# Performance work log

Measured on AMD Instinct MI355X. Metric: run time of the kernel, lower is better.

Reference implementation:

```python
import jax, jax.numpy as jnp
import numpy as np

T_DIFF = 1000.0
LN_EPS = 1e-5


def _lin(x, w, b):
    return jnp.matmul(x, w.T) + b


def _ln(x, g, b):
    m = jnp.mean(x, axis=-1, keepdims=True)
    v = jnp.mean((x - m) ** 2, axis=-1, keepdims=True)
    return (x - m) / jnp.sqrt(v + LN_EPS) * g + b


def _pos_lin(x, w, b):
    return jnp.matmul(x, jax.nn.softplus(w).T) + b


def _gamma(t, g_l1_w, g_l1_b, g_l2_w, g_l2_b, g_l3_w, g_l3_b, gamma_0, gamma_1):
    def gtilde(u):
        l1 = _pos_lin(u, g_l1_w, g_l1_b)
        return l1 + _pos_lin(jax.nn.sigmoid(_pos_lin(l1, g_l2_w, g_l2_b)), g_l3_w, g_l3_b)
    g0, g1, gt = gtilde(jnp.zeros_like(t)), gtilde(jnp.ones_like(t)), gtilde(t)
    return gamma_0 + (gamma_1 - gamma_0) * (gt - g0) / (g1 - g0)


def _pair_dist(a):
    # safe pairwise euclidean distances, (B,N,N,1)
    diff = a[:, :, None, :] - a[:, None, :, :]
    d2 = jnp.sum(diff * diff, axis=-1, keepdims=True)
    return diff, jnp.sqrt(jnp.maximum(d2, 1e-12)), d2


def _egc_layer(x, h, x0, p):
    _, d0, _ = _pair_dist(x0)                      # original distances
    diff, dist, d2 = _pair_dist(x)                 # current distances (pre-LN x)
    h = _ln(h, p['lnh_g'], p['lnh_b'])
    x = _ln(x, p['lnx_g'], p['lnx_b'])
    B, N, F = h.shape
    h_i = jnp.broadcast_to(h[:, :, None, :], (B, N, N, F))
    h_j = jnp.broadcast_to(h[:, None, :, :], (B, N, N, F))
    einp = jnp.concatenate([h_i, h_j, d2, d0], axis=-1)  # (B,N,N,2F+2)
    m = jax.nn.silu(_lin(einp, p['edg1_w'], p['edg1_b']))
    m = jax.nn.silu(_lin(m, p['edg2_w'], p['edg2_b']))
    e = jax.nn.sigmoid(_lin(m, p['edgi_w'], p['edgi_b']))
    e = e * (1.0 - jnp.eye(N, dtype=e.dtype)[None, :, :, None])
    m_agg = jnp.sum(e * m, axis=2)                 # sum over j -> (B,N,F)
    hn = jax.nn.silu(_lin(jnp.concatenate([h, m_agg], axis=-1), p['node1_w'], p['node1_b']))
    hn = h + _lin(hn, p['node2_w'], p['node2_b'])
    cw = jax.nn.silu(_lin(einp, p['cor1_w'], p['cor1_b']))
    cw = jax.nn.silu(_lin(cw, p['cor2_w'], p['cor2_b']))
    cw = _lin(cw, p['cor3_w'], p['cor3_b'])        # (B,N,N,1)
    x_next = x + jnp.sum(cw * (diff / (dist + 1.0)), axis=2)
    return x_next, hn


def setup_inputs() -> dict:
    key = jax.random.key(0)
    ks = iter(jax.random.split(key, 64))
    B, N, H, L = 8, 192, 32, 4
    d = {}
    d['xyz_atom_species'] = jax.random.normal(next(ks), (B, N, 4), jnp.float32)
    d['pdf'] = jax.random.normal(next(ks), (B, 3000), jnp.float32)
    d['t'] = jax.random.uniform(next(ks), (B,), jnp.float32) * T_DIFF

    def w(k, shape):
        fan_in = shape[-1]
        return jax.random.normal(k, shape, jnp.float32) / np.sqrt(fan_in)

    d['emb_in_w'] = w(next(ks), (H, 12)); d['emb_in_b'] = jnp.zeros((H,), jnp.float32)
    d['emb_out_w'] = w(next(ks), (1, H)); d['emb_out_b'] = jnp.zeros((1,), jnp.float32)
    d['x_out_w'] = w(next(ks), (3, 3)); d['x_out_b'] = jnp.zeros((3,), jnp.float32)
    d['pdf_w'] = w(next(ks), (10, 3000)); d['pdf_b'] = jnp.zeros((10,), jnp.float32)
    d['g_l1_w'] = w(next(ks), (1, 1)); d['g_l1_b'] = jnp.zeros((1,), jnp.float32)
    d['g_l2_w'] = w(next(ks), (1024, 1)); d['g_l2_b'] = jnp.zeros((1024,), jnp.float32)
    d['g_l3_w'] = w(next(ks), (1, 1024)); d['g_l3_b'] = jnp.zeros((1,), jnp.float32)
    d['gamma_0'] = jnp.array([-5.0], jnp.float32)
    d['gamma_1'] = jnp.array([10.0], jnp.float32)
    d['lnh_g'] = jnp.ones((L, H), jnp.float32); d['lnh_b'] = jnp.zeros((L, H), jnp.float32)
    d['lnx_g'] = jnp.ones((L, 3), jnp.float32); d['lnx_b'] = jnp.zeros((L, 3), jnp.float32)
    d['edg1_w'] = w(next(ks), (L, H, 2 * H + 2)); d['edg1_b'] = jnp.zeros((L, H), jnp.float32)
    d['edg2_w'] = w(next(ks), (L, H, H)); d['edg2_b'] = jnp.zeros((L, H), jnp.float32)
    d['edgi_w'] = w(next(ks), (L, 1, H)); d['edgi_b'] = jnp.zeros((L, 1), jnp.float32)
    d['node1_w'] = w(next(ks), (L, H, 2 * H)); d['node1_b'] = jnp.zeros((L, H), jnp.float32)
    d['node2_w'] = w(next(ks), (L, H, H)); d['node2_b'] = jnp.zeros((L, H), jnp.float32)
    d['cor1_w'] = w(next(ks), (L, H, 2 * H + 2)); d['cor1_b'] = jnp.zeros((L, H), jnp.float32)
    d['cor2_w'] = w(next(ks), (L, H, H)); d['cor2_b'] = jnp.zeros((L, H), jnp.float32)
    d['cor3_w'] = w(next(ks), (L, 1, H)); d['cor3_b'] = jnp.zeros((L, 1), jnp.float32)
    return d


def reference(xyz_atom_species, pdf, t, emb_in_w, emb_in_b, emb_out_w, emb_out_b,
              x_out_w, x_out_b, pdf_w, pdf_b, g_l1_w, g_l1_b, g_l2_w, g_l2_b,
              g_l3_w, g_l3_b, gamma_0, gamma_1, lnh_g, lnh_b, lnx_g, lnx_b,
              edg1_w, edg1_b, edg2_w, edg2_b, edgi_w, edgi_b, node1_w, node1_b,
              node2_w, node2_b, cor1_w, cor1_b, cor2_w, cor2_b, cor3_w, cor3_b):
    B, N, _ = xyz_atom_species.shape
    h = xyz_atom_species[:, :, 3:4]                # (B,N,1)
    x = xyz_atom_species[:, :, :3]
    x0 = x
    tn = (t / T_DIFF)[:, None]                     # (B,1)
    t_emb = _gamma(tn, g_l1_w, g_l1_b, g_l2_w, g_l2_b, g_l3_w, g_l3_b, gamma_0, gamma_1)
    pdf_emb = _lin(pdf, pdf_w, pdf_b)              # (B,10)
    h = jnp.concatenate([
        h,
        jnp.broadcast_to(t_emb[:, None, :], (B, N, 1)),
        jnp.broadcast_to(pdf_emb[:, None, :], (B, N, 10)),
    ], axis=-1)
    h = _lin(h, emb_in_w, emb_in_b)                # (B,N,32)
    for l in range(4):
        p = dict(lnh_g=lnh_g[l], lnh_b=lnh_b[l], lnx_g=lnx_g[l], lnx_b=lnx_b[l],
                 edg1_w=edg1_w[l], edg1_b=edg1_b[l], edg2_w=edg2_w[l], edg2_b=edg2_b[l],
                 edgi_w=edgi_w[l], edgi_b=edgi_b[l], node1_w=node1_w[l], node1_b=node1_b[l],
                 node2_w=node2_w[l], node2_b=node2_b[l], cor1_w=cor1_w[l], cor1_b=cor1_b[l],
                 cor2_w=cor2_w[l], cor2_b=cor2_b[l], cor3_w=cor3_w[l], cor3_b=cor3_b[l])
        x, h = _egc_layer(x, h, x0, p)
    h = _lin(h, emb_out_w, emb_out_b)
    x = _lin(x, x_out_w, x_out_b) - x0
    return jnp.concatenate([x, h], axis=-1)        # (B,N,4)
```

## Files before the change

kernel.cpp:

```cpp
#include <hip/hip_runtime.h>
#include <hip/hip_bf16.h>
#include <math.h>

#define BATCH 8
#define NATOMS 192

using short8 = __attribute__((ext_vector_type(8))) short;
using f32x4  = __attribute__((ext_vector_type(4))) float;

__device__ __forceinline__ float fast_rcp(float x){ return __builtin_amdgcn_rcpf(x); }
__device__ __forceinline__ float sigmoid_f(float x){ return fast_rcp(1.0f+__expf(-x)); }
__device__ __forceinline__ float silu_f(float x){ return x*fast_rcp(1.0f+__expf(-x)); }
__device__ __forceinline__ float softplus_f(float x){ return fmaxf(x,0.0f)+log1pf(expf(-fabsf(x))); }
__device__ __forceinline__ unsigned short f2bf(float x){
  __hip_bfloat16 h = __float2bfloat16(x);
  return __builtin_bit_cast(unsigned short, h);
}

__device__ __forceinline__ float wave_sum(float v){
  v += __shfl_xor(v, 1);
  v += __shfl_xor(v, 2);
  v += __shfl_xor(v, 4);
  v += __shfl_xor(v, 8);
  v += __shfl_xor(v, 16);
  v += __shfl_xor(v, 32);
  return v;
}
__device__ __forceinline__ float sum32(float v){
  v += __shfl_xor(v, 1);
  v += __shfl_xor(v, 2);
  v += __shfl_xor(v, 4);
  v += __shfl_xor(v, 8);
  v += __shfl_xor(v, 16);
  return v;
}

struct KP {
  const float *xyz, *pdf, *t;
  const float *emb_in_w, *emb_in_b, *emb_out_w, *emb_out_b, *x_out_w, *x_out_b;
  const float *pdf_w, *pdf_b;
  const float *g1w, *g1b, *g2w, *g2b, *g3w, *g3b, *gamma0, *gamma1;
  const float *lnhg, *lnhb, *lnxg, *lnxb;
  const float *e1w, *e1b, *e2w, *e2b, *eiw, *eib;
  const float *n1w, *n1b, *n2w, *n2b;
  const float *c1w, *c1b, *c2w, *c2b, *c3w, *c3b;
  float *temb, *pdfe;
  unsigned short *e2wb, *c2wb;
  float *hln0, *hln1, *ue0, *uc0, *vep0, *vcp0, *ue1, *uc1, *vep1, *vcp1;
  float *xb0, *xb1;
  float *out;
};

__global__ __launch_bounds__(128) void k_prelude(KP P)
{
  __shared__ float s_sm[8];
  const int bx = blockIdx.x, tid = threadIdx.x;
  const int wv = tid >> 6, ln = tid & 63;

  if (bx < 80){
    const int b = bx / 10, o = bx % 10;
    const float* pb = P.pdf + b*3000;
    const float* wb = P.pdf_w + o*3000;
    float p = 0.f;
    for (int k = tid; k < 3000; k += 128) p = fmaf(pb[k], wb[k], p);
    p = wave_sum(p);
    if (ln == 0) s_sm[wv] = p;
    __syncthreads();
    if (tid == 0) P.pdfe[b*10 + o] = s_sm[0] + s_sm[1] + P.pdf_b[o];
  } else if (bx < 88){
    const int b = bx - 80;
    const float w1 = softplus_f(P.g1w[0]);
    const float b1 = P.g1b[0];
    const float tn = P.t[b] * (1.0f/1000.0f);
    const float l1_0 = b1;
    const float l1_1 = w1 + b1;
    const float l1_t = fmaf(w1, tn, b1);
    float a0 = 0.f, a1 = 0.f, at = 0.f;
    for (int k = tid; k < 1024; k += 128){
      float w2 = softplus_f(P.g2w[k]);
      float bb = P.g2b[k];
      float w3 = softplus_f(P.g3w[k]);
      a0 += sigmoid_f(fmaf(w2, l1_0, bb)) * w3;
      a1 += sigmoid_f(fmaf(w2, l1_1, bb)) * w3;
      at += sigmoid_f(fmaf(w2, l1_t, bb)) * w3;
    }
    float vals[3] = {a0, a1, at};
#pragma unroll
    for (int r = 0; r < 3; ++r){
      float v = wave_sum(vals[r]);
      if (ln == 0) s_sm[r*2 + wv] = v;
    }
    __syncthreads();
    if (tid == 0){
      const float b3 = P.g3b[0];
      const float g0  = l1_0 + s_sm[0] + s_sm[1] + b3;
      const float g1v = l1_1 + s_sm[2] + s_sm[3] + b3;
      const float gt  = l1_t + s_sm[4] + s_sm[5] + b3;
      P.temb[b] = P.gamma0[0] + (P.gamma1[0] - P.gamma0[0]) * (gt - g0) / (g1v - g0);
    }
  } else {
    const int g = (bx - 88)*128 + tid;
    P.e2wb[g] = f2bf(P.e2w[g]);
    P.c2wb[g] = f2bf(P.c2w[g]);
  }
}

__global__ __launch_bounds__(128) void k_embed(KP P)
{
  __shared__ float s_hl[32];
  const int nid = blockIdx.x;
  const int tid = threadIdx.x;
  const int wv = tid >> 6, ln = tid & 63;
  const int b = nid / NATOMS;
  if (tid < 32){
    const int f = tid;
    const float* w = P.emb_in_w + f*12;
    float a = P.emb_in_b[f];
    a = fmaf(P.xyz[nid*4 + 3], w[0], a);
    a = fmaf(P.temb[b], w[1], a);
    const float* pe = P.pdfe + b*10;
#pragma unroll
    for (int q = 0; q < 10; ++q) a = fmaf(pe[q], w[2+q], a);
    const float m = sum32(a) * (1.0f/32.0f);
    const float d = a - m;
    const float v = sum32(d*d);
    const float r = rsqrtf(v*(1.0f/32.0f) + 1e-5f);
    const float hlv = fmaf(d*r, P.lnhg[f], P.lnhb[f]);
    s_hl[f] = hlv;
    P.hln0[(size_t)nid*32 + f] = hlv;
    if (f < 3) P.xb0[(size_t)nid*3 + f] = P.xyz[nid*4 + f];
  }
  __syncthreads();
  if (ln < 32){
    const int f = ln;
    const float* W = ((wv == 0) ? P.e1w : P.c1w) + f*66;
    float sv = ((wv == 0) ? P.e1b : P.c1b)[f], su = 0.f;
#pragma unroll
    for (int k = 0; k < 32; ++k){ sv = fmaf(s_hl[k], W[k], sv); su = fmaf(s_hl[k], W[32+k], su); }
    if (wv == 0){ P.vep0[(size_t)nid*32 + f] = sv; P.ue0[(size_t)nid*32 + f] = su; }
    else        { P.vcp0[(size_t)nid*32 + f] = sv; P.uc0[(size_t)nid*32 + f] = su; }
  }
}

__global__ __launch_bounds__(128, 4) void k_layer(KP P, int l, int last,
    const float* __restrict__ xcur, float* __restrict__ xnxt,
    const float* __restrict__ hlnC, float* __restrict__ hlnN,
    const float* __restrict__ ueC, const float* __restrict__ ucC,
    const float* __restrict__ vepC, const float* __restrict__ vcpC,
    float* __restrict__ ueN, float* __restrict__ ucN,
    float* __restrict__ vepN, float* __restrict__ vcpN)
{
  __shared__ float s_geo[192][6];
  __shared__ float s_hv[32];
  __shared__ float s_mg[32];
  __shared__ float s_n1[32];
  __shared__ float s_hl[32];

  const int nid = blockIdx.x;
  const int b = nid / NATOMS;
  const int i = nid - b*NATOMS;
  const int base = b*NATOMS;
  const int tid = threadIdx.x;
  const int wv = tid >> 6, lane = tid & 63;
  const int n16 = lane & 15, quad = lane >> 4;

  {
    const float* xi_p = xcur + (size_t)nid*3;
    const float xi0 = xi_p[0], xi1 = xi_p[1], xi2 = xi_p[2];
    const float* x0i = P.xyz + (size_t)nid*4;
    const float q0i = x0i[0], q1i = x0i[1], q2i = x0i[2];
    for (int j = tid; j < NATOMS; j += 128){
      const float* xj_p = xcur + (size_t)(base + j)*3;
      const float dfx = xi0 - xj_p[0], dfy = xi1 - xj_p[1], dfz = xi2 - xj_p[2];
      const float d2 = dfx*dfx + dfy*dfy + dfz*dfz;
      const float dist = sqrtf(fmaxf(d2, 1e-12f));
      const float* x0j = P.xyz + (size_t)(base + j)*4;
      const float q0 = q0i - x0j[0], q1 = q1i - x0j[1], q2 = q2i - x0j[2];
      const float d0 = sqrtf(fmaxf(q0*q0 + q1*q1 + q2*q2, 1e-12f));
      s_geo[j][0] = dfx; s_geo[j][1] = dfy; s_geo[j][2] = dfz;
      s_geo[j][3] = d2;  s_geo[j][4] = d0;  s_geo[j][5] = dist;
    }
  }

  const float* e1wl = ((wv == 0) ? P.e1w : P.c1w) + l*2112;
  const float* vp   = ((wv == 0) ? vepC : vcpC) + (size_t)nid*32;
  const float* uu   = (wv == 0) ? ueC : ucC;
  const unsigned short* w2b = ((wv == 0) ? P.e2wb : P.c2wb) + l*1024;

  float vp8[8], wA[8], wB[8];
#pragma unroll
  for (int q = 0; q < 8; ++q){
    const int k = quad*8 + q;
    vp8[q] = vp[k];
    wA[q] = e1wl[k*66 + 64];
    wB[q] = e1wl[k*66 + 65];
  }
  const short8 wb0 = *(const short8*)(w2b + n16*32 + quad*8);
  const short8 wb1 = *(const short8*)(w2b + 512 + n16*32 + quad*8);

  float q0s, q1s, q2s, q3s, q4s;
  if (wv == 0){
    q0s = P.e2b[l*32 + n16]; q1s = P.e2b[l*32 + 16 + n16];
    q2s = P.eiw[l*32 + n16]; q3s = P.eiw[l*32 + 16 + n16]; q4s = P.eib[l];
  } else {
    q0s = P.c2b[l*32 + n16]; q1s = P.c2b[l*32 + 16 + n16];
    q2s = P.c3w[l*32 + n16]; q3s = P.c3w[l*32 + 16 + n16]; q4s = P.c3b[l];
  }

  __syncthreads();

  float ma0 = 0.f, ma1 = 0.f;
  float px = 0.f, py = 0.f, pz = 0.f;

#pragma unroll 4
  for (int t = 0; t < 12; ++t){
    const int j = t*16 + n16;
    const float d2 = s_geo[j][3], d0 = s_geo[j][4];
    const float* ur = uu + (size_t)(base + j)*32 + quad*8;
    const f32x4 ua = *(const f32x4*)ur;
    const f32x4 ub = *(const f32x4*)(ur + 4);
    short8 a;
#pragma unroll
    for (int q = 0; q < 4; ++q)
      a[q] = (short)f2bf(silu_f(fmaf(d2, wA[q], fmaf(d0, wB[q], vp8[q] + ua[q]))));
#pragma unroll
    for (int q = 0; q < 4; ++q)
      a[4+q] = (short)f2bf(silu_f(fmaf(d2, wA[4+q], fmaf(d0, wB[4+q], vp8[4+q] + ub[q]))));

    const f32x4 z = {0.f, 0.f, 0.f, 0.f};
    const f32x4 A0 = __builtin_amdgcn_mfma_f32_16x16x32_bf16(a, wb0, z, 0, 0, 0);
    const f32x4 A1 = __builtin_amdgcn_mfma_f32_16x16x32_bf16(a, wb1, z, 0, 0, 0);

    if (wv == 0){
      float m20[4], m21[4], g[4];
#pragma unroll
      for (int r = 0; r < 4; ++r){
        m20[r] = silu_f(A0[r] + q0s);
        m21[r] = silu_f(A1[r] + q1s);
        g[r] = m20[r]*q2s + m21[r]*q3s;
      }
#pragma unroll
      for (int r = 0; r < 4; ++r){
        g[r] += __shfl_xor(g[r], 1);
        g[r] += __shfl_xor(g[r], 2);
        g[r] += __shfl_xor(g[r], 4);
        g[r] += __shfl_xor(g[r], 8);
      }
#pragma unroll
      for (int r = 0; r < 4; ++r){
        const int jglob = t*16 + quad*4 + r;
        const float e = (jglob == i) ? 0.0f : sigmoid_f(g[r] + q4s);
        ma0 = fmaf(e, m20[r], ma0);
        ma1 = fmaf(e, m21[r], ma1);
      }
    } else {
      float g[4];
#pragma unroll
      for (int r = 0; r < 4; ++r)
        g[r] = silu_f(A0[r] + q0s)*q2s + silu_f(A1[r] + q1s)*q3s;
#pragma unroll
      for (int r = 0; r < 4; ++r){
        g[r] += __shfl_xor(g[r], 1);
        g[r] += __shfl_xor(g[r], 2);
        g[r] += __shfl_xor(g[r], 4);
        g[r] += __shfl_xor(g[r], 8);
      }
#pragma unroll
      for (int r = 0; r < 4; ++r){
        const int jj = t*16 + quad*4 + r;
        const float s = (g[r] + q4s) * fast_rcp(s_geo[jj][5] + 1.0f);
        px = fmaf(s, s_geo[jj][0], px);
        py = fmaf(s, s_geo[jj][1], py);
        pz = fmaf(s, s_geo[jj][2], pz);
      }
    }
  }

  if (wv == 0){
    ma0 += __shfl_xor(ma0, 16); ma0 += __shfl_xor(ma0, 32);
    ma1 += __shfl_xor(ma1, 16); ma1 += __shfl_xor(ma1, 32);
    if (lane < 16){ s_mg[lane] = ma0; s_mg[16 + lane] = ma1; }
  } else {
    px += __shfl_xor(px, 16); px += __shfl_xor(px, 32);
    py += __shfl_xor(py, 16); py += __shfl_xor(py, 32);
    pz += __shfl_xor(pz, 16); pz += __shfl_xor(pz, 32);
    if (lane < 32) s_hv[lane] = hlnC[(size_t)nid*32 + lane];
  }
  __syncthreads();

  if (wv == 0){
    if (lane < 32){
      const int f = lane;
      float a = P.n1b[l*32 + f];
      const float* w1 = P.n1w + l*2048 + f*64;
#pragma unroll
      for (int k = 0; k < 32; ++k) a = fmaf(s_hv[k], w1[k], a);
#pragma unroll
      for (int k = 0; k < 32; ++k) a = fmaf(s_mg[k], w1[32+k], a);
      s_n1[f] = silu_f(a);
    }
  } else {
    const float* xr = xcur + (size_t)nid*3;
    const float x0 = xr[0], x1 = xr[1], x2 = xr[2];
    const float mx = (x0 + x1 + x2) * (1.0f/3.0f);
    const float v0 = x0-mx, v1 = x1-mx, v2 = x2-mx;
    const float r = rsqrtf((v0*v0 + v1*v1 + v2*v2)*(1.0f/3.0f) + 1e-5f);
    const float xn0 = fmaf((x0 - mx)*r, P.lnxg[l*3+0], P.lnxb[l*3+0]) + px;
    const float xn1 = fmaf((x1 - mx)*r, P.lnxg[l*3+1], P.lnxb[l*3+1]) + py;
    const float xn2 = fmaf((x2 - mx)*r, P.lnxg[l*3+2], P.lnxb[l*3+2]) + pz;
    if (!last){
      if (lane == 0){
        float* xo = xnxt + (size_t)nid*3;
        xo[0] = xn0; xo[1] = xn1; xo[2] = xn2;
      }
    } else if (lane < 3){
      float o = P.x_out_b[lane];
      o = fmaf(xn0, P.x_out_w[lane*3 + 0], o);
      o = fmaf(xn1, P.x_out_w[lane*3 + 1], o);
      o = fmaf(xn2, P.x_out_w[lane*3 + 2], o);
      P.out[(size_t)nid*4 + lane] = o - P.xyz[(size_t)nid*4 + lane];
    }
  }
  __syncthreads();

  if (wv == 0 && lane < 32){
    const int f = lane;
    float o = P.n2b[l*32 + f];
    const float* w2 = P.n2w + l*1024 + f*32;
#pragma unroll
    for (int k = 0; k < 32; ++k) o = fmaf(s_n1[k], w2[k], o);
    const float ho = s_hv[f] + o;
    if (last){
      float hp = sum32(ho * P.emb_out_w[f]);
      if (f == 0) P.out[(size_t)nid*4 + 3] = hp + P.emb_out_b[0];
    } else {
      const int nx = l + 1;
      const float m = sum32(ho) * (1.0f/32.0f);
      const float d = ho - m;
      const float v = sum32(d*d);
      const float r = rsqrtf(v*(1.0f/32.0f) + 1e-5f);
      const float hlv = fmaf(d*r, P.lnhg[nx*32 + f], P.lnhb[nx*32 + f]);
      s_hl[f] = hlv;
      hlnN[(size_t)nid*32 + f] = hlv;
    }
  }
  if (!last){
    __syncthreads();
    if (lane < 32){
      const int f = lane;
      const int nx = l + 1;
      const float* W = ((wv == 0) ? P.e1w : P.c1w) + nx*2112 + f*66;
      float sv = ((wv == 0) ? P.e1b : P.c1b)[nx*32 + f], su = 0.f;
#pragma unroll
      for (int k = 0; k < 32; ++k){ sv = fmaf(s_hl[k], W[k], sv); su = fmaf(s_hl[k], W[32+k], su); }
      if (wv == 0){ vepN[(size_t)nid*32 + f] = sv; ueN[(size_t)nid*32 + f] = su; }
      else        { vcpN[(size_t)nid*32 + f] = sv; ucN[(size_t)nid*32 + f] = su; }
    }
  }
}

extern "C" void kernel_launch(void* const* d_in, const int* in_sizes, int n_in,
                              void* d_out, int out_size, void* d_ws, size_t ws_size,
                              hipStream_t stream)
{
  const int NTOT = BATCH*NATOMS;
  float* ws   = (float*)d_ws;

  KP P;
  P.xyz      = (const float*)d_in[0];
  P.pdf      = (const float*)d_in[1];
  P.t        = (const float*)d_in[2];
  P.emb_in_w = (const float*)d_in[3];
  P.emb_in_b = (const float*)d_in[4];
  P.emb_out_w= (const float*)d_in[5];
  P.emb_out_b= (const float*)d_in[6];
  P.x_out_w  = (const float*)d_in[7];
  P.x_out_b  = (const float*)d_in[8];
  P.pdf_w    = (const float*)d_in[9];
  P.pdf_b    = (const float*)d_in[10];
  P.g1w      = (const float*)d_in[11];
  P.g1b      = (const float*)d_in[12];
  P.g2w      = (const float*)d_in[13];
  P.g2b      = (const float*)d_in[14];
  P.g3w      = (const float*)d_in[15];
  P.g3b      = (const float*)d_in[16];
  P.gamma0   = (const float*)d_in[17];
  P.gamma1   = (const float*)d_in[18];
  P.lnhg     = (const float*)d_in[19];
  P.lnhb     = (const float*)d_in[20];
  P.lnxg     = (const float*)d_in[21];
  P.lnxb     = (const float*)d_in[22];
  P.e1w      = (const float*)d_in[23];
  P.e1b      = (const float*)d_in[24];
  P.e2w      = (const float*)d_in[25];
  P.e2b      = (const float*)d_in[26];
  P.eiw      = (const float*)d_in[27];
  P.eib      = (const float*)d_in[28];
  P.n1w      = (const float*)d_in[29];
  P.n1b      = (const float*)d_in[30];
  P.n2w      = (const float*)d_in[31];
  P.n2b      = (const float*)d_in[32];
  P.c1w      = (const float*)d_in[33];
  P.c1b      = (const float*)d_in[34];
  P.c2w      = (const float*)d_in[35];
  P.c2b      = (const float*)d_in[36];
  P.c3w      = (const float*)d_in[37];
  P.c3b      = (const float*)d_in[38];

  P.temb = ws;
  P.pdfe = ws + 8;
  P.e2wb = (unsigned short*)(ws + 96);
  P.c2wb = P.e2wb + 4096;
  float* p = ws + 96 + 4096;
  P.hln0 = p; p += NTOT*32;
  P.hln1 = p; p += NTOT*32;
  P.ue0  = p; p += NTOT*32;
  P.uc0  = p; p += NTOT*32;
  P.vep0 = p; p += NTOT*32;
  P.vcp0 = p; p += NTOT*32;
  P.ue1  = p; p += NTOT*32;
  P.uc1  = p; p += NTOT*32;
  P.vep1 = p; p += NTOT*32;
  P.vcp1 = p; p += NTOT*32;
  P.xb0  = p; p += NTOT*3;
  P.xb1  = p; p += NTOT*3;
  P.out  = (float*)d_out;

  k_prelude<<<120, 128, 0, stream>>>(P);
  k_embed<<<NTOT, 128, 0, stream>>>(P);

  float* xcur = P.xb0; float* xnxt = P.xb1;
  float* hlnC = P.hln0; float* hlnN = P.hln1;
  float* ueC = P.ue0;  float* ucC = P.uc0;  float* vepC = P.vep0; float* vcpC = P.vcp0;
  float* ueN = P.ue1;  float* ucN = P.uc1;  float* vepN = P.vep1; float* vcpN = P.vcp1;
  for (int l = 0; l < 4; ++l){
    k_layer<<<NTOT, 128, 0, stream>>>(P, l, (l == 3) ? 1 : 0, xcur, xnxt,
        hlnC, hlnN, ueC, ucC, vepC, vcpC, ueN, ucN, vepN, vcpN);
    float* tp;
    tp = hlnC; hlnC = hlnN; hlnN = tp;
    tp = ueC;  ueC  = ueN;  ueN  = tp;
    tp = ucC;  ucC  = ucN;  ucN  = tp;
    tp = vepC; vepC = vepN; vepN = tp;
    tp = vcpC; vcpC = vcpN; vcpN = tp;
    tp = xcur; xcur = xnxt; xnxt = tp;
  }
}
```

Before: 254.0 us.

## Split each node's edge loop across two waves per MLP and transpose MFMA operands

The layer kernel now launches 256 threads per node, using two waves each for the edge MLP and the coordinate MLP. Each wave handles alternating 16-neighbour tiles, and the partial sums are combined through shared memory. The MFMA operands are swapped so each lane holds one neighbour's outputs, which reduces the per-row shuffle reductions to two cross-quad shuffles per tile. The aim is more latency hiding and a shorter serial loop per node, at the cost of larger blocks, extra shared-memory reductions and possibly lower occupancy.

```diff
diff --git a/kernel.cpp b/kernel.cpp
--- a/kernel.cpp
+++ b/kernel.cpp
@@ -32,6 +32,13 @@
   v += __shfl_xor(v, 4);
   v += __shfl_xor(v, 8);
   v += __shfl_xor(v, 16);
+  return v;
+}
+__device__ __forceinline__ float sum16(float v){
+  v += __shfl_xor(v, 1);
+  v += __shfl_xor(v, 2);
+  v += __shfl_xor(v, 4);
+  v += __shfl_xor(v, 8);
   return v;
 }
 
@@ -142,7 +149,7 @@
   }
 }
 
-__global__ __launch_bounds__(128, 4) void k_layer(KP P, int l, int last,
+__global__ __launch_bounds__(256, 4) void k_layer(KP P, int l, int last,
     const float* __restrict__ xcur, float* __restrict__ xnxt,
     const float* __restrict__ hlnC, float* __restrict__ hlnN,
     const float* __restrict__ ueC, const float* __restrict__ ucC,
@@ -151,8 +158,9 @@
     float* __restrict__ vepN, float* __restrict__ vcpN)
 {
   __shared__ float s_geo[192][6];
+  __shared__ float s_mgp[2][32];
+  __shared__ float s_pxp[2][4];
   __shared__ float s_hv[32];
-  __shared__ float s_mg[32];
   __shared__ float s_n1[32];
   __shared__ float s_hl[32];
 
@@ -163,13 +171,15 @@
   const int tid = threadIdx.x;
   const int wv = tid >> 6, lane = tid & 63;
   const int n16 = lane & 15, quad = lane >> 4;
+  const int is_edge = (wv < 2);
+  const int half = wv & 1;
 
   {
     const float* xi_p = xcur + (size_t)nid*3;
     const float xi0 = xi_p[0], xi1 = xi_p[1], xi2 = xi_p[2];
     const float* x0i = P.xyz + (size_t)nid*4;
     const float q0i = x0i[0], q1i = x0i[1], q2i = x0i[2];
-    for (int j = tid; j < NATOMS; j += 128){
+    for (int j = tid; j < NATOMS; j += 256){
       const float* xj_p = xcur + (size_t)(base + j)*3;
       const float dfx = xi0 - xj_p[0], dfy = xi1 - xj_p[1], dfz = xi2 - xj_p[2];
       const float d2 = dfx*dfx + dfy*dfy + dfz*dfz;
@@ -182,10 +192,13 @@
     }
   }
 
-  const float* e1wl = ((wv == 0) ? P.e1w : P.c1w) + l*2112;
-  const float* vp   = ((wv == 0) ? vepC : vcpC) + (size_t)nid*32;
-  const float* uu   = (wv == 0) ? ueC : ucC;
-  const unsigned short* w2b = ((wv == 0) ? P.e2wb : P.c2wb) + l*1024;
+  const float* e1wl = (is_edge ? P.e1w : P.c1w) + l*2112;
+  const float* vp   = (is_edge ? vepC : vcpC) + (size_t)nid*32;
+  const float* uu   = is_edge ? ueC : ucC;
+  const unsigned short* w2b = (is_edge ? P.e2wb : P.c2wb) + l*1024;
+  const float* bias2 = (is_edge ? P.e2b : P.c2b) + l*32;
+  const float* wout  = (is_edge ? P.eiw : P.c3w) + l*32;
+  const float  bout  = (is_edge ? P.eib : P.c3b)[l];
 
   float vp8[8], wA[8], wB[8];
 #pragma unroll
@@ -198,22 +211,23 @@
   const short8 wb0 = *(const short8*)(w2b + n16*32 + quad*8);
   const short8 wb1 = *(const short8*)(w2b + 512 + n16*32 + quad*8);
 
-  float q0s, q1s, q2s, q3s, q4s;
-  if (wv == 0){
-    q0s = P.e2b[l*32 + n16]; q1s = P.e2b[l*32 + 16 + n16];
-    q2s = P.eiw[l*32 + n16]; q3s = P.eiw[l*32 + 16 + n16]; q4s = P.eib[l];
-  } else {
-    q0s = P.c2b[l*32 + n16]; q1s = P.c2b[l*32 + 16 + n16];
-    q2s = P.c3w[l*32 + n16]; q3s = P.c3w[l*32 + 16 + n16]; q4s = P.c3b[l];
+  float bA[4], bB[4], wAo[4], wBo[4];
+#pragma unroll
+  for (int r = 0; r < 4; ++r){
+    bA[r]  = bias2[quad*4 + r];
+    bB[r]  = bias2[16 + quad*4 + r];
+    wAo[r] = wout[quad*4 + r];
+    wBo[r] = wout[16 + quad*4 + r];
   }
 
   __syncthreads();
 
-  float ma0 = 0.f, ma1 = 0.f;
+  float acc0[4] = {0.f,0.f,0.f,0.f};
+  float acc1[4] = {0.f,0.f,0.f,0.f};
   float px = 0.f, py = 0.f, pz = 0.f;
 
-#pragma unroll 4
-  for (int t = 0; t < 12; ++t){
+#pragma unroll 3
+  for (int t = half; t < 12; t += 2){
     const int j = t*16 + n16;
     const float d2 = s_geo[j][3], d0 = s_geo[j][4];
     const float* ur = uu + (size_t)(base + j)*32 + quad*8;
@@ -228,63 +242,55 @@
       a[4+q] = (short)f2bf(silu_f(fmaf(d2, wA[4+q], fmaf(d0, wB[4+q], vp8[4+q] + ub[q]))));
 
     const f32x4 z = {0.f, 0.f, 0.f, 0.f};
-    const f32x4 A0 = __builtin_amdgcn_mfma_f32_16x16x32_bf16(a, wb0, z, 0, 0, 0);
-    const f32x4 A1 = __builtin_amdgcn_mfma_f32_16x16x32_bf16(a, wb1, z, 0, 0, 0);
-
-    if (wv == 0){
-      float m20[4], m21[4], g[4];
+    const f32x4 A0 = __builtin_amdgcn_mfma_f32_16x16x32_bf16(wb0, a, z, 0, 0, 0);
+    const f32x4 A1 = __builtin_amdgcn_mfma_f32_16x16x32_bf16(wb1, a, z, 0, 0, 0);
+
+    float m20[4], m21[4];
+#pragma unroll
+    for (int r = 0; r < 4; ++r){
+      m20[r] = silu_f(A0[r] + bA[r]);
+      m21[r] = silu_f(A1[r] + bB[r]);
+    }
+    float gp = 0.f;
+#pragma unroll
+    for (int r = 0; r < 4; ++r) gp += m20[r]*wAo[r] + m21[r]*wBo[r];
+    gp += __shfl_xor(gp, 16);
+    gp += __shfl_xor(gp, 32);
+
+    if (is_edge){
+      const float e = (j == i) ? 0.0f : sigmoid_f(gp + bout);
 #pragma unroll
       for (int r = 0; r < 4; ++r){
-        m20[r] = silu_f(A0[r] + q0s);
-        m21[r] = silu_f(A1[r] + q1s);
-        g[r] = m20[r]*q2s + m21[r]*q3s;
-      }
-#pragma unroll
-      for (int r = 0; r < 4; ++r){
-        g[r] += __shfl_xor(g[r], 1);
-        g[r] += __shfl_xor(g[r], 2);
-        g[r] += __shfl_xor(g[r], 4);
-        g[r] += __shfl_xor(g[r], 8);
-      }
-#pragma unroll
-      for (int r = 0; r < 4; ++r){
-        const int jglob = t*16 + quad*4 + r;
-        const float e = (jglob == i) ? 0.0f : sigmoid_f(g[r] + q4s);
-        ma0 = fmaf(e, m20[r], ma0);
-        ma1 = fmaf(e, m21[r], ma1);
+        acc0[r] = fmaf(e, m20[r], acc0[r]);
+        acc1[r] = fmaf(e, m21[r], acc1[r]);
       }
     } else {
-      float g[4];
-#pragma unroll
-      for (int r = 0; r < 4; ++r)
-        g[r] = silu_f(A0[r] + q0s)*q2s + silu_f(A1[r] + q1s)*q3s;
+      const float s = (gp + bout) * fast_rcp(s_geo[j][5] + 1.0f);
+      px = fmaf(s, s_geo[j][0], px);
+      py = fmaf(s, s_geo[j][1], py);
+      pz = fmaf(s, s_geo[j][2], pz);
+    }
+  }
+
+  if (is_edge){
+#pragma unroll
+    for (int r = 0; r < 4; ++r){
+      acc0[r] = sum16(acc0[r]);
+      acc1[r] = sum16(acc1[r]);
+    }
+    if (n16 == 0){
 #pragma unroll
       for (int r = 0; r < 4; ++r){
-        g[r] += __shfl_xor(g[r], 1);
-        g[r] += __shfl_xor(g[r], 2);
-        g[r] += __shfl_xor(g[r], 4);
-        g[r] += __shfl_xor(g[r], 8);
+        s_mgp[half][quad*4 + r] = acc0[r];
+        s_mgp[half][16 + quad*4 + r] = acc1[r];
       }
-#pragma unroll
-      for (int r = 0; r < 4; ++r){
-        const int jj = t*16 + quad*4 + r;
-        const float s = (g[r] + q4s) * fast_rcp(s_geo[jj][5] + 1.0f);
-        px = fmaf(s, s_geo[jj][0], px);
-        py = fmaf(s, s_geo[jj][1], py);
-        pz = fmaf(s, s_geo[jj][2], pz);
-      }
-    }
-  }
-
-  if (wv == 0){
-    ma0 += __shfl_xor(ma0, 16); ma0 += __shfl_xor(ma0, 32);
-    ma1 += __shfl_xor(ma1, 16); ma1 += __shfl_xor(ma1, 32);
-    if (lane < 16){ s_mg[lane] = ma0; s_mg[16 + lane] = ma1; }
+    }
   } else {
-    px += __shfl_xor(px, 16); px += __shfl_xor(px, 32);
-    py += __shfl_xor(py, 16); py += __shfl_xor(py, 32);
-    pz += __shfl_xor(pz, 16); pz += __shfl_xor(pz, 32);
-    if (lane < 32) s_hv[lane] = hlnC[(size_t)nid*32 + lane];
+    px = sum16(px); py = sum16(py); pz = sum16(pz);
+    if (lane == 0){
+      s_pxp[half][0] = px; s_pxp[half][1] = py; s_pxp[half][2] = pz;
+    }
+    if (half == 1 && lane < 32) s_hv[lane] = hlnC[(size_t)nid*32 + lane];
   }
   __syncthreads();
 
@@ -296,28 +302,32 @@
 #pragma unroll
       for (int k = 0; k < 32; ++k) a = fmaf(s_hv[k], w1[k], a);
 #pragma unroll
-      for (int k = 0; k < 32; ++k) a = fmaf(s_mg[k], w1[32+k], a);
+      for (int k = 0; k < 32; ++k) a = fmaf(s_mgp[0][k] + s_mgp[1][k], w1[32+k], a);
       s_n1[f] = silu_f(a);
     }
-  } else {
+  } else if (wv == 1){
+    const float tx = s_pxp[0][0] + s_pxp[1][0];
+    const float ty = s_pxp[0][1] + s_pxp[1][1];
+    const float tz = s_pxp[0][2] + s_pxp[1][2];
     const float* xr = xcur + (size_t)nid*3;
     const float x0 = xr[0], x1 = xr[1], x2 = xr[2];
     const float mx = (x0 + x1 + x2) * (1.0f/3.0f);
     const float v0 = x0-mx, v1 = x1-mx, v2 = x2-mx;
     const float r = rsqrtf((v0*v0 + v1*v1 + v2*v2)*(1.0f/3.0f) + 1e-5f);
-    const float xn0 = fmaf((x0 - mx)*r, P.lnxg[l*3+0], P.lnxb[l*3+0]) + px;
-    const float xn1 = fmaf((x1 - mx)*r, P.lnxg[l*3+1], P.lnxb[l*3+1]) + py;
-    const float xn2 = fmaf((x2 - mx)*r, P.lnxg[l*3+2], P.lnxb[l*3+2]) + pz;
+    const float xn0 = fmaf((x0 - mx)*r, P.lnxg[l*3+0], P.lnxb[l*3+0]) + tx;
+    const float xn1 = fmaf((x1 - mx)*r, P.lnxg[l*3+1], P.lnxb[l*3+1]) + ty;
+    const float xn2 = fmaf((x2 - mx)*r, P.lnxg[l*3+2], P.lnxb[l*3+2]) + tz;
     if (!last){
       if (lane == 0){
         float* xo = xnxt + (size_t)nid*3;
         xo[0] = xn0; xo[1] = xn1; xo[2] = xn2;
       }
     } else if (lane < 3){
+      const float xn[3] = {xn0, xn1, xn2};
       float o = P.x_out_b[lane];
-      o = fmaf(xn0, P.x_out_w[lane*3 + 0], o);
-      o = fmaf(xn1, P.x_out_w[lane*3 + 1], o);
-      o = fmaf(xn2, P.x_out_w[lane*3 + 2], o);
+      o = fmaf(xn[0], P.x_out_w[lane*3 + 0], o);
+      o = fmaf(xn[1], P.x_out_w[lane*3 + 1], o);
+      o = fmaf(xn[2], P.x_out_w[lane*3 + 2], o);
       P.out[(size_t)nid*4 + lane] = o - P.xyz[(size_t)nid*4 + lane];
     }
   }
@@ -346,7 +356,7 @@
   }
   if (!last){
     __syncthreads();
-    if (lane < 32){
+    if (wv < 2 && lane < 32){
       const int f = lane;
       const int nx = l + 1;
       const float* W = ((wv == 0) ? P.e1w : P.c1w) + nx*2112 + f*66;
@@ -434,7 +444,7 @@
   float* ueC = P.ue0;  float* ucC = P.uc0;  float* vepC = P.vep0; float* vcpC = P.vcp0;
   float* ueN = P.ue1;  float* ucN = P.uc1;  float* vepN = P.vep1; float* vcpN = P.vcp1;
   for (int l = 0; l < 4; ++l){
-    k_layer<<<NTOT, 128, 0, stream>>>(P, l, (l == 3) ? 1 : 0, xcur, xnxt,
+    k_layer<<<NTOT, 256, 0, stream>>>(P, l, (l == 3) ? 1 : 0, xcur, xnxt,
         hlnC, hlnN, ueC, ucC, vepC, vcpC, ueN, ucN, vepN, vcpN);
     float* tp;
     tp = hlnC; hlnC = hlnN; hlnN = tp;
```

Result: faster. 235.6 us (-7.3%).
